# Kernel optimization log

Hardware: AMD Instinct MI355X
Metric: run time of the kernel (lower is better)

## Reference

```python
import jax, jax.numpy as jnp
import numpy as np

C_IN = 128
C_OUT = 128
N_EDGE_TYPE = 7
N_NODE_TYPE = 7
AVG_DEGREE = 7
NUMD = 524288                 # nodes at depth d (multiple of 8)
LNUMD = 32768                 # leaf nodes at depth d-1
NNUM_DM1 = LNUMD + NUMD // 8  # 98304 nodes at depth d-1
PREFIX = 16384                # nodes at depths < d-1 kept in x
N_TOTAL_X = PREFIX + LNUMD + NUMD   # 573440
N_CONV = PREFIX + NNUM_DM1          # 114688 nodes seen by GraphConv
N_EDGES = N_CONV * AVG_DEGREE       # 802816


def setup_inputs() -> dict:
    key = jax.random.key(0)
    ks = jax.random.split(key, 6)
    x = jax.random.normal(ks[0], (N_TOTAL_X, C_IN), dtype=jnp.float32)
    # exactly LNUMD True entries (98304 = 3 * 32768), deterministic
    leaf_mask = (jnp.arange(NNUM_DM1) % 3) == 0
    edge_index = jax.random.randint(ks[1], (2, N_EDGES), 0, N_CONV)
    edge_type = jax.random.randint(ks[2], (N_EDGES,), 0, N_EDGE_TYPE)
    node_type = jax.random.randint(ks[3], (N_CONV,), 0, N_NODE_TYPE)
    w_down = jax.random.normal(ks[4], (C_IN, C_IN, 8), dtype=jnp.float32) * 0.02
    w_conv = jax.random.normal(
        ks[5], (N_EDGE_TYPE * (C_IN + N_NODE_TYPE), C_OUT), dtype=jnp.float32) * 0.02
    return dict(x=x, leaf_mask=leaf_mask, edge_index=edge_index,
                edge_type=edge_type, node_type=node_type,
                w_down=w_down, w_conv=w_conv)


def _graph_conv(x, edge_index, edge_type, node_type, w_conv):
    # x: [N, C]; augment with one-hot node type (n_node_type > 1)
    one_hot = jax.nn.one_hot(node_type, N_NODE_TYPE, dtype=x.dtype)
    xa = jnp.concatenate([x, one_hot], axis=1)          # [N, C+T]
    row, col = edge_index[0], edge_index[1]
    bucket = row * N_EDGE_TYPE + edge_type              # [E]
    # scatter-add neighbor features into per-(node, edge_type) buckets
    col_data = jax.ops.segment_sum(xa[col], bucket,
                                   num_segments=x.shape[0] * N_EDGE_TYPE)
    # [N, n_edge_type*(C+T)] @ [n_edge_type*(C+T), C_out]
    return col_data.reshape(x.shape[0], -1) @ w_conv


def reference(x, leaf_mask, edge_index, edge_type, node_type, w_down, w_conv):
    # Downsample: merge groups of 8 child nodes with a (C, C*8) weight
    xd = x[-NUMD:].reshape(-1, C_IN * 8)                # [NUMD/8, C*8]
    outd = xd @ w_down.reshape(C_IN, C_IN * 8).T        # [NUMD/8, C]
    # Masked scatter assembly: out[leaf_mask] = leaf feats, out[~mask] = outd
    x_leaf = x[-LNUMD - NUMD:-NUMD]                     # [LNUMD, C]
    li = jnp.cumsum(leaf_mask) - 1                      # position among leaves
    ni = jnp.cumsum(~leaf_mask) - 1                     # position among non-leaves
    merged = jnp.where(leaf_mask[:, None], x_leaf[li], outd[ni])  # [NNUM_DM1, C]
    out = jnp.concatenate([x[:-NUMD - LNUMD], merged], axis=0)    # [N_CONV, C]
    return _graph_conv(out, edge_index, edge_type, node_type, w_conv)
```

## Files before the change

kernel.cpp:

```cpp
#include <hip/hip_runtime.h>
#include <stdint.h>

#define C_IN 128
#define NUMD 524288
#define LNUMD 32768
#define NNUM_DM1 (LNUMD + NUMD/8)
#define PREFIX 16384
#define N_CONV (PREFIX + NNUM_DM1)
#define N_EDGES (N_CONV * 7)
#define ND8 (NUMD/8)
#define CAP 32
#define EG 12

#define COPY_BLK ((PREFIX+LNUMD)*32/256)
#define PREPW_N (114688 + 6272 + 131072)
#define PREPW_BLK ((PREPW_N + 255)/256)
#define ZERO_BLK 308
#define DOWN_BLK (ND8/64)
#define SCAT_BLK (N_EDGES/256)

typedef __attribute__((ext_vector_type(8))) short short8;
typedef __attribute__((ext_vector_type(4))) float f32x4;

__device__ inline ushort f2b(float f){
  union { float f; uint32_t u; } v; v.f = f;
  uint32_t r = v.u + 0x7fffu + ((v.u >> 16) & 1u);
  return (ushort)(r >> 16);
}
__device__ inline float b2f_lo(uint32_t u){ union { uint32_t u; float f; } v; v.u = u << 16; return v.f; }
__device__ inline float b2f_hi(uint32_t u){ union { uint32_t u; float f; } v; v.u = u & 0xffff0000u; return v.f; }

#define BAR_LGKM() do { \
    asm volatile("s_waitcnt lgkmcnt(0)" ::: "memory"); \
    __builtin_amdgcn_s_barrier(); \
    asm volatile("" ::: "memory"); \
  } while(0)

__global__ void k_prep(const float* __restrict__ x, const float* __restrict__ wconv,
                       const float* __restrict__ wdown,
                       ushort* __restrict__ xconv, ushort* __restrict__ w16y,
                       ushort* __restrict__ wbias, ushort* __restrict__ wd16,
                       int* __restrict__ cnt){
  const int bid = blockIdx.x;
  if (bid < COPY_BLK){
    int gid = bid*256 + threadIdx.x;
    int row = gid >> 5, seg = (gid & 31) * 4;
    int srow, drow;
    if (row < PREFIX){ srow = row; drow = row; }
    else { int k = row - PREFIX; srow = PREFIX + k; drow = PREFIX + 3*k; }
    const float4 f = *(const float4*)(x + (size_t)srow*C_IN + seg);
    ushort4 o; o.x=f2b(f.x); o.y=f2b(f.y); o.z=f2b(f.z); o.w=f2b(f.w);
    *(ushort4*)(xconv + (size_t)drow*C_IN + seg) = o;
  } else if (bid < COPY_BLK + PREPW_BLK){
    int gid = (bid - COPY_BLK)*256 + threadIdx.x;
    if (gid < 114688){
      int t = gid >> 14, rem = gid & 16383;
      int o = rem >> 7, k = rem & 127;
      w16y[gid] = f2b(wconv[(size_t)(t*135 + k)*128 + o]);
    } else if (gid < 120960){
      int q = gid - 114688;
      int t = q / 896, rem = q % 896;
      int n = rem >> 7, o = rem & 127;
      wbias[q] = f2b(wconv[(size_t)(t*135 + 128 + n)*128 + o]);
    } else if (gid < PREPW_N){
      int i = gid - 120960;
      wd16[i] = f2b(wdown[i]);
    }
  } else {
    int gid = (bid - COPY_BLK - PREPW_BLK)*256 + threadIdx.x;
    int4 z = {0,0,0,0};
    *(int4*)(cnt + gid*4) = z;
  }
}

__global__ __launch_bounds__(256, 2) void k_sd(const int* __restrict__ ei, const int* __restrict__ et,
    int* __restrict__ cnt, int* __restrict__ bucket, unsigned char* __restrict__ used,
    const float* __restrict__ x, const ushort* __restrict__ wd16, ushort* __restrict__ xconv){
  const int bid = blockIdx.x;
  if (bid >= DOWN_BLK){
    int e = (bid - DOWN_BLK)*256 + threadIdx.x;
    int r = ei[e], c = ei[N_EDGES + e], t = et[e];
    int key = c*7 + t;
    int pos = atomicAdd(&cnt[r], 1);
    if (pos < CAP) bucket[r*CAP + pos] = key;
    used[key] = 1;
    return;
  }
  __shared__ ushort Ab[2][64*128];
  const int tid = threadIdx.x;
  const int n0 = bid * 64;
  const float* xd = x + (size_t)(PREFIX+LNUMD)*C_IN;

  const int w = tid >> 6, lane = tid & 63;
  const int rg = w >> 1, cg = w & 1;
  const int arow = lane & 15, kgrp = lane >> 4;

  const int prow = (lane >> 5);
  const int pcol = (lane & 31) * 4;

  float4 pf[8];
  #pragma unroll
  for (int j=0;j<8;j++)
    pf[j] = *(const float4*)(xd + (size_t)(n0 + (w*8+j)*2 + prow)*1024 + 0*128 + pcol);

  f32x4 acc[2][4];
  #pragma unroll
  for (int mf=0;mf<2;mf++){
    #pragma unroll
    for (int cf=0;cf<4;cf++) acc[mf][cf] = (f32x4){0.f,0.f,0.f,0.f};
  }

  #pragma unroll
  for (int c = 0; c < 8; ++c){
    short8 breg[4][4];
    #pragma unroll
    for (int kf=0;kf<4;kf++){
      #pragma unroll
      for (int cf=0;cf<4;cf++){
        int o = cg*64 + cf*16 + arow;
        breg[kf][cf] = *(const short8*)(wd16 + (size_t)o*1024 + c*128 + kf*32 + kgrp*8);
      }
    }
    #pragma unroll
    for (int j=0;j<8;j++){
      int row = (w*8+j)*2 + prow;
      uint lo = (uint)f2b(pf[j].x) | ((uint)f2b(pf[j].y)<<16);
      uint hi = (uint)f2b(pf[j].z) | ((uint)f2b(pf[j].w)<<16);
      int slot = (lane & 31) >> 1;
      int sw = slot ^ ((row & 7) << 1);
      uint2 u; u.x = lo; u.y = hi;
      *(uint2*)((char*)&Ab[c&1][0] + row*256 + sw*16 + (lane&1)*8) = u;
    }
    if (c < 7){
      #pragma unroll
      for (int j=0;j<8;j++)
        pf[j] = *(const float4*)(xd + (size_t)(n0 + (w*8+j)*2 + prow)*1024 + (c+1)*128 + pcol);
    }
    BAR_LGKM();

    #pragma unroll
    for (int kf=0;kf<4;kf++){
      #pragma unroll
      for (int mf=0;mf<2;mf++){
        int row = rg*32 + mf*16 + arow;
        int sw = (kf*4 + kgrp) ^ ((arow & 7) << 1);
        short8 a = *(const short8*)((const char*)&Ab[c&1][0] + row*256 + sw*16);
        #pragma unroll
        for (int cf=0;cf<4;cf++)
          acc[mf][cf] = __builtin_amdgcn_mfma_f32_16x16x32_bf16(a, breg[kf][cf], acc[mf][cf], 0,0,0);
      }
    }
  }

  #pragma unroll
  for (int mf = 0; mf < 2; ++mf){
    #pragma unroll
    for (int cf = 0; cf < 4; ++cf){
      #pragma unroll
      for (int j = 0; j < 4; ++j){
        int rl = rg*32 + mf*16 + kgrp*4 + j;
        int n = n0 + rl;
        int i = 3*(n>>1) + 1 + (n&1);
        xconv[(size_t)(PREFIX + i)*C_IN + cg*64 + cf*16 + arow] = f2b(acc[mf][cf][j]);
      }
    }
  }
}

__global__ __launch_bounds__(512) void k_y(const ushort* __restrict__ xconv,
    const ushort* __restrict__ w16y, const ushort* __restrict__ wbias,
    const int* __restrict__ ntype, const unsigned char* __restrict__ used,
    ushort* __restrict__ Y){
  __shared__ ushort As[128*128];
  __shared__ ushort bsh[6272];
  __shared__ int nts[128];
  __shared__ uint usedw[224];
  const int tid = threadIdx.x;
  const int tile = blockIdx.x;
  const unsigned char* usedb = (const unsigned char*)usedw;

  {
    int row = tid >> 2;
    int c0 = (tid & 3) * 4;
    const ushort* src = xconv + ((size_t)tile*128 + row)*128;
    #pragma unroll
    for (int i=0;i<4;i++){
      int c16 = c0 + i;
      uint4 v = *(const uint4*)(src + c16*8);
      *(uint4*)&As[row*128 + ((c16 ^ (row & 7))*8)] = v;
    }
  }
  for (int i = tid; i < 3136; i += 512) ((uint*)bsh)[i] = ((const uint*)wbias)[i];
  if (tid < 128) nts[tid] = ntype[tile*128 + tid];
  if (tid < 224) usedw[tid] = ((const uint*)(used + (size_t)tile*896))[tid];
  __syncthreads();

  const int w = tid >> 6, l = tid & 63;
  const int mg = w >> 2, nc = w & 3;
  const int arow = l & 15, kgrp = l >> 4;
  const int obase = nc*32 + arow;

  for (int t = 0; t < 7; ++t){
    f32x4 acc[4][2];
    #pragma unroll
    for (int mf=0;mf<4;mf++){ acc[mf][0]=(f32x4){0,0,0,0}; acc[mf][1]=(f32x4){0,0,0,0}; }
    const ushort* wt = w16y + t*16384;
    #pragma unroll
    for (int kf = 0; kf < 4; ++kf){
      const int kof = kf*32 + kgrp*8;
      short8 b0 = *(const short8*)(wt + (size_t)obase*128 + kof);
      short8 b1 = *(const short8*)(wt + (size_t)(obase+16)*128 + kof);
      #pragma unroll
      for (int mf = 0; mf < 4; ++mf){
        int row = mg*64 + mf*16 + arow;
        int c16 = (kf*4 + kgrp) ^ (row & 7);
        short8 a = *(const short8*)&As[row*128 + c16*8];
        acc[mf][0] = __builtin_amdgcn_mfma_f32_16x16x32_bf16(a, b0, acc[mf][0], 0,0,0);
        acc[mf][1] = __builtin_amdgcn_mfma_f32_16x16x32_bf16(a, b1, acc[mf][1], 0,0,0);
      }
    }
    #pragma unroll
    for (int mf = 0; mf < 4; ++mf){
      #pragma unroll
      for (int j = 0; j < 4; ++j){
        int rl = mg*64 + mf*16 + (l>>4)*4 + j;
        if (usedb[rl*7 + t]){
          int ntv = nts[rl];
          size_t grow = ((size_t)(tile*128 + rl)*7 + t)*128;
          int bb = (t*7 + ntv)*128;
          Y[grow + obase]      = f2b(acc[mf][0][j] + b2f_lo((uint)bsh[bb + obase]));
          Y[grow + obase + 16] = f2b(acc[mf][1][j] + b2f_lo((uint)bsh[bb + obase + 16]));
        }
      }
    }
  }
}

__global__ __launch_bounds__(256) void k_gather(const int* __restrict__ cnt,
    const int* __restrict__ bucket, const ushort* __restrict__ Y, float* __restrict__ out){
  const int tid = threadIdx.x;
  const int slot = tid >> 4, lane = tid & 15;
  const int v = blockIdx.x*16 + slot;
  const int n = min(cnt[v], CAP);
  const int* brow = bucket + (size_t)v*CAP;
  float acc[8] = {0.f,0.f,0.f,0.f,0.f,0.f,0.f,0.f};

  int m[EG]; uint4 d[EG];
  const int nb = min(n, EG);
  #pragma unroll
  for (int i=0;i<EG;i++) if (i < nb) m[i] = brow[i];
  #pragma unroll
  for (int i=0;i<EG;i++) if (i < nb)
    d[i] = *(const uint4*)(Y + (size_t)m[i]*C_IN + lane*8);
  #pragma unroll
  for (int i=0;i<EG;i++){
    if (i < nb){
      acc[0] += b2f_lo(d[i].x); acc[1] += b2f_hi(d[i].x);
      acc[2] += b2f_lo(d[i].y); acc[3] += b2f_hi(d[i].y);
      acc[4] += b2f_lo(d[i].z); acc[5] += b2f_hi(d[i].z);
      acc[6] += b2f_lo(d[i].w); acc[7] += b2f_hi(d[i].w);
    }
  }
  for (int e = EG; e < n; e += 4){
    int n4 = min(n - e, 4);
    int m4[4]; uint4 d4[4];
    #pragma unroll
    for (int i=0;i<4;i++) if (i < n4) m4[i] = brow[e + i];
    #pragma unroll
    for (int i=0;i<4;i++) if (i < n4)
      d4[i] = *(const uint4*)(Y + (size_t)m4[i]*C_IN + lane*8);
    #pragma unroll
    for (int i=0;i<4;i++){
      if (i < n4){
        acc[0] += b2f_lo(d4[i].x); acc[1] += b2f_hi(d4[i].x);
        acc[2] += b2f_lo(d4[i].y); acc[3] += b2f_hi(d4[i].y);
        acc[4] += b2f_lo(d4[i].z); acc[5] += b2f_hi(d4[i].z);
        acc[6] += b2f_lo(d4[i].w); acc[7] += b2f_hi(d4[i].w);
      }
    }
  }
  float4 o0; o0.x=acc[0]; o0.y=acc[1]; o0.z=acc[2]; o0.w=acc[3];
  float4 o1; o1.x=acc[4]; o1.y=acc[5]; o1.z=acc[6]; o1.w=acc[7];
  float* dst = out + (size_t)v*C_IN + lane*8;
  *(float4*)dst = o0;
  *(float4*)(dst + 4) = o1;
}

extern "C" void kernel_launch(void* const* d_in, const int* in_sizes, int n_in,
                              void* d_out, int out_size, void* d_ws, size_t ws_size,
                              hipStream_t stream){
  const float* x     = (const float*)d_in[0];
  const int*   ei    = (const int*)d_in[2];
  const int*   et    = (const int*)d_in[3];
  const int*   nt    = (const int*)d_in[4];
  const float* wdown = (const float*)d_in[5];
  const float* wconv = (const float*)d_in[6];
  float* out = (float*)d_out;

  char* p = (char*)d_ws;
  ushort* xconv = (ushort*)p; p += (size_t)N_CONV*C_IN*2;
  ushort* wd16  = (ushort*)p; p += (size_t)128*1024*2;
  ushort* w16y  = (ushort*)p; p += (size_t)114688*2;
  ushort* wbias = (ushort*)p; p += 16384;
  int* cnt      = (int*)p;    p += (size_t)N_CONV*4;
  unsigned char* used = (unsigned char*)p; p += 802816;
  int* bucket   = (int*)p;    p += (size_t)N_CONV*CAP*4;
  ushort* Y     = (ushort*)p;

  k_prep<<<COPY_BLK + PREPW_BLK + ZERO_BLK, 256, 0, stream>>>(x, wconv, wdown, xconv, w16y, wbias, wd16, cnt);
  k_sd<<<DOWN_BLK + SCAT_BLK, 256, 0, stream>>>(ei, et, cnt, bucket, used, x, wd16, xconv);
  k_y<<<N_CONV/128, 512, 0, stream>>>(xconv, w16y, wbias, nt, used, Y);
  k_gather<<<N_CONV/16, 256, 0, stream>>>(cnt, bucket, Y, out);
}
```

Baseline: 307.6 us.

## Replace LDS-staged downsample GEMM with per-wave register-direct MFMA tiles

```diff
diff --git a/kernel.cpp b/kernel.cpp
--- a/kernel.cpp
+++ b/kernel.cpp
@@ -29,12 +29,6 @@
 }
 __device__ inline float b2f_lo(uint32_t u){ union { uint32_t u; float f; } v; v.u = u << 16; return v.f; }
 __device__ inline float b2f_hi(uint32_t u){ union { uint32_t u; float f; } v; v.u = u & 0xffff0000u; return v.f; }
-
-#define BAR_LGKM() do { \
-    asm volatile("s_waitcnt lgkmcnt(0)" ::: "memory"); \
-    __builtin_amdgcn_s_barrier(); \
-    asm volatile("" ::: "memory"); \
-  } while(0)
 
 __global__ void k_prep(const float* __restrict__ x, const float* __restrict__ wconv,
                        const float* __restrict__ wdown,
@@ -73,7 +67,7 @@
   }
 }
 
-__global__ __launch_bounds__(256, 2) void k_sd(const int* __restrict__ ei, const int* __restrict__ et,
+__global__ void k_sd(const int* __restrict__ ei, const int* __restrict__ et,
     int* __restrict__ cnt, int* __restrict__ bucket, unsigned char* __restrict__ used,
     const float* __restrict__ x, const ushort* __restrict__ wd16, ushort* __restrict__ xconv){
   const int bid = blockIdx.x;
@@ -86,83 +80,54 @@
     used[key] = 1;
     return;
   }
-  __shared__ ushort Ab[2][64*128];
   const int tid = threadIdx.x;
-  const int n0 = bid * 64;
+  const int w = tid >> 6, lane = tid & 63;
+  const int arow = lane & 15, kg = lane >> 4;
+  const int n0 = (bid*4 + w) * 16;
   const float* xd = x + (size_t)(PREFIX+LNUMD)*C_IN;
-
-  const int w = tid >> 6, lane = tid & 63;
-  const int rg = w >> 1, cg = w & 1;
-  const int arow = lane & 15, kgrp = lane >> 4;
-
-  const int prow = (lane >> 5);
-  const int pcol = (lane & 31) * 4;
-
-  float4 pf[8];
-  #pragma unroll
-  for (int j=0;j<8;j++)
-    pf[j] = *(const float4*)(xd + (size_t)(n0 + (w*8+j)*2 + prow)*1024 + 0*128 + pcol);
-
-  f32x4 acc[2][4];
-  #pragma unroll
-  for (int mf=0;mf<2;mf++){
-    #pragma unroll
-    for (int cf=0;cf<4;cf++) acc[mf][cf] = (f32x4){0.f,0.f,0.f,0.f};
-  }
-
-  #pragma unroll
-  for (int c = 0; c < 8; ++c){
-    short8 breg[4][4];
-    #pragma unroll
-    for (int kf=0;kf<4;kf++){
+  const float*  asrc = xd  + (size_t)(n0 + arow)*1024 + kg*8;
+  const ushort* bsrc = wd16 + (size_t)arow*1024 + kg*8;
+
+  f32x4 acc[8];
+  #pragma unroll
+  for (int s=0;s<8;s++) acc[s] = (f32x4){0.f,0.f,0.f,0.f};
+
+  float4 af[2][2];
+  short8 bb[2][8];
+  af[0][0] = *(const float4*)(asrc);
+  af[0][1] = *(const float4*)(asrc + 4);
+  #pragma unroll
+  for (int s=0;s<8;s++) bb[0][s] = *(const short8*)(bsrc + s*16*1024);
+
+  #pragma unroll
+  for (int c = 0; c < 32; ++c){
+    const int cur = c & 1, nxt = cur ^ 1;
+    if (c < 31){
+      af[nxt][0] = *(const float4*)(asrc + (c+1)*32);
+      af[nxt][1] = *(const float4*)(asrc + (c+1)*32 + 4);
       #pragma unroll
-      for (int cf=0;cf<4;cf++){
-        int o = cg*64 + cf*16 + arow;
-        breg[kf][cf] = *(const short8*)(wd16 + (size_t)o*1024 + c*128 + kf*32 + kgrp*8);
-      }
-    }
-    #pragma unroll
-    for (int j=0;j<8;j++){
-      int row = (w*8+j)*2 + prow;
-      uint lo = (uint)f2b(pf[j].x) | ((uint)f2b(pf[j].y)<<16);
-      uint hi = (uint)f2b(pf[j].z) | ((uint)f2b(pf[j].w)<<16);
-      int slot = (lane & 31) >> 1;
-      int sw = slot ^ ((row & 7) << 1);
-      uint2 u; u.x = lo; u.y = hi;
-      *(uint2*)((char*)&Ab[c&1][0] + row*256 + sw*16 + (lane&1)*8) = u;
-    }
-    if (c < 7){
-      #pragma unroll
-      for (int j=0;j<8;j++)
-        pf[j] = *(const float4*)(xd + (size_t)(n0 + (w*8+j)*2 + prow)*1024 + (c+1)*128 + pcol);
-    }
-    BAR_LGKM();
-
-    #pragma unroll
-    for (int kf=0;kf<4;kf++){
-      #pragma unroll
-      for (int mf=0;mf<2;mf++){
-        int row = rg*32 + mf*16 + arow;
-        int sw = (kf*4 + kgrp) ^ ((arow & 7) << 1);
-        short8 a = *(const short8*)((const char*)&Ab[c&1][0] + row*256 + sw*16);
-        #pragma unroll
-        for (int cf=0;cf<4;cf++)
-          acc[mf][cf] = __builtin_amdgcn_mfma_f32_16x16x32_bf16(a, breg[kf][cf], acc[mf][cf], 0,0,0);
-      }
-    }
-  }
-
-  #pragma unroll
-  for (int mf = 0; mf < 2; ++mf){
-    #pragma unroll
-    for (int cf = 0; cf < 4; ++cf){
-      #pragma unroll
-      for (int j = 0; j < 4; ++j){
-        int rl = rg*32 + mf*16 + kgrp*4 + j;
-        int n = n0 + rl;
-        int i = 3*(n>>1) + 1 + (n&1);
-        xconv[(size_t)(PREFIX + i)*C_IN + cg*64 + cf*16 + arow] = f2b(acc[mf][cf][j]);
-      }
+      for (int s=0;s<8;s++) bb[nxt][s] = *(const short8*)(bsrc + s*16*1024 + (c+1)*32);
+    }
+    short8 a;
+    uint4 pk;
+    pk.x = (uint)f2b(af[cur][0].x) | ((uint)f2b(af[cur][0].y)<<16);
+    pk.y = (uint)f2b(af[cur][0].z) | ((uint)f2b(af[cur][0].w)<<16);
+    pk.z = (uint)f2b(af[cur][1].x) | ((uint)f2b(af[cur][1].y)<<16);
+    pk.w = (uint)f2b(af[cur][1].z) | ((uint)f2b(af[cur][1].w)<<16);
+    a = *(short8*)&pk;
+    #pragma unroll
+    for (int s=0;s<8;s++)
+      acc[s] = __builtin_amdgcn_mfma_f32_16x16x32_bf16(a, bb[cur][s], acc[s], 0,0,0);
+  }
+
+  #pragma unroll
+  for (int s=0;s<8;s++){
+    int col = s*16 + arow;
+    #pragma unroll
+    for (int j=0;j<4;j++){
+      int n = n0 + kg*4 + j;
+      int i = 3*(n>>1) + 1 + (n&1);
+      xconv[(size_t)(PREFIX + i)*C_IN + col] = f2b(acc[s][j]);
     }
   }
 }
```

Result: slower. 368.7 us (+19.9%).
